# Kernel tuning notes

Hardware: AMD Instinct MI355X
Metric: run time of the kernel (lower is better)

## Reference

```python
import jax, jax.numpy as jnp
import numpy as np

SIGMA = 1e-4            # df_cone_height
PENALIZE_OUTSIDE = True
POINT2PLANE = False
EPS = 1e-12


def _tri_frame(tris):
    """tris: [..., 3, 3] -> centroid c [...,3], unit normal n [...,3], circum-radius r [...]."""
    v0, v1, v2 = tris[..., 0, :], tris[..., 1, :], tris[..., 2, :]
    c = (v0 + v1 + v2) / 3.0
    n = jnp.cross(v1 - v0, v2 - v0)
    n = n / jnp.maximum(jnp.linalg.norm(n, axis=-1, keepdims=True), EPS)
    r = jnp.sqrt(jnp.maximum(jnp.maximum(jnp.sum((v0 - c) ** 2, -1),
                                         jnp.sum((v1 - c) ** 2, -1)),
                             jnp.sum((v2 - c) ** 2, -1)))
    return c, n, r


def _cone_psi(points, c, n, r):
    """Conic distance-field value of each point w.r.t. a triangle cone.
    points: [..., 3, 3] (3 vertices), c/n: [..., 3], r: [...]. Returns [..., 3].
    Cone: axis = triangle normal through centroid, base radius r, height SIGMA.
    """
    u = points - c[..., None, :]                       # [..., 3v, 3]
    h = jnp.einsum('...vk,...k->...v', u, n)           # signed height along normal
    rho = jnp.linalg.norm(u - h[..., None] * n[..., None, :], axis=-1)  # radial dist
    radial = jnp.maximum(1.0 - rho / jnp.maximum(r[..., None], EPS), 0.0)
    if PENALIZE_OUTSIDE:
        axial = jnp.maximum(SIGMA - h, 0.0)            # also penalize thin band above surface
    else:
        axial = jnp.maximum(-h, 0.0)                   # only true penetration (below surface)
    return radial * axial


def setup_inputs() -> dict:
    key = jax.random.key(0)
    B, V, F, C = 8, 10475, 20908, 262144
    k1, k2, k3, k4 = jax.random.split(key, 4)
    vertices = jax.random.normal(k1, (B, V, 3), dtype=jnp.float32)
    faces = jax.random.randint(k2, (F, 3), 0, V)
    idxs = jax.random.randint(k3, (B, C, 2), 0, F)
    invalid = jax.random.uniform(k4, (B, C)) < 0.2     # padded (-1) collision slots
    collision_idxs = jnp.where(invalid[..., None], -1, idxs)
    return {"vertices": vertices, "faces": faces, "collision_idxs": collision_idxs}


def reference(vertices, faces, collision_idxs):
    # triangles: [B, F, 3, 3]
    triangles = jnp.take(vertices, faces, axis=1)
    recv_idx = collision_idxs[..., 0]                  # [B, C]
    intr_idx = collision_idxs[..., 1]
    valid = (recv_idx >= 0) & (intr_idx >= 0)
    # irregular gather of colliding triangle pairs: [B, C, 3, 3]
    recv = jnp.take_along_axis(triangles, jnp.clip(recv_idx, 0)[..., None, None], axis=1)
    intr = jnp.take_along_axis(triangles, jnp.clip(intr_idx, 0)[..., None, None], axis=1)
    rc, rn, rr = _tri_frame(recv)
    ic, inn, ir = _tri_frame(intr)
    psi_i = _cone_psi(intr, rc, rn, rr)                # intruder verts in receiver cone [B,C,3]
    psi_r = _cone_psi(recv, ic, inn, ir)               # receiver verts in intruder cone
    # penetration vector per vertex = -psi * n (unit normal) -> squared norm = psi^2
    per_pair = jnp.sum(psi_i ** 2 + psi_r ** 2, axis=-1)  # [B, C]
    loss = jnp.sum(jnp.where(valid, per_pair, 0.0), axis=1)  # [B]
    # original returns 0.0 when no collision index is >= 0
    return jnp.where(jnp.any(valid), loss, jnp.zeros_like(loss))
```

## Files before the change

kernel.cpp:

```cpp
#include <hip/hip_runtime.h>

#define SIGMA_C 1e-4f
#define EPS_C   1e-12f
#define GPT     4

struct V3 { float x, y, z; };
typedef float v2f __attribute__((ext_vector_type(2)));

__device__ __forceinline__ V3 v3sub(V3 a, V3 b) { return {a.x - b.x, a.y - b.y, a.z - b.z}; }
__device__ __forceinline__ float v3dot(V3 a, V3 b) { return a.x * b.x + a.y * b.y + a.z * b.z; }
__device__ __forceinline__ V3 v3cross(V3 a, V3 b) {
    return {a.y * b.z - a.z * b.y,
            a.z * b.x - a.x * b.z,
            a.x * b.y - a.y * b.x};
}
__device__ __forceinline__ int imax0(int x) { return x > 0 ? x : 0; }

__device__ __forceinline__ void tri_frame(const V3 v[3], V3& c, V3& n, float& r) {
    const float third = 1.0f / 3.0f;
    c.x = (v[0].x + v[1].x + v[2].x) * third;
    c.y = (v[0].y + v[1].y + v[2].y) * third;
    c.z = (v[0].z + v[1].z + v[2].z) * third;
    V3 e1 = v3sub(v[1], v[0]);
    V3 e2 = v3sub(v[2], v[0]);
    n = v3cross(e1, e2);
    float nn = sqrtf(v3dot(n, n));
    float inv = 1.0f / fmaxf(nn, EPS_C);
    n.x *= inv; n.y *= inv; n.z *= inv;
    V3 d0 = v3sub(v[0], c), d1 = v3sub(v[1], c), d2 = v3sub(v[2], c);
    float m = fmaxf(fmaxf(v3dot(d0, d0), v3dot(d1, d1)), v3dot(d2, d2));
    r = sqrtf(m);
}

__device__ __forceinline__ float cone_psi2(const V3 p[3], V3 c, V3 n, float r) {
    float inv_r = 1.0f / fmaxf(r, EPS_C);
    float s = 0.0f;
#pragma unroll
    for (int i = 0; i < 3; ++i) {
        V3 u = v3sub(p[i], c);
        float h = v3dot(u, n);
        V3 w = {u.x - h * n.x, u.y - h * n.y, u.z - h * n.z};
        float rho = sqrtf(v3dot(w, w));
        float radial = fmaxf(1.0f - rho * inv_r, 0.0f);
        float axial = fmaxf(SIGMA_C - h, 0.0f);
        float psi = radial * axial;
        s += psi * psi;
    }
    return s;
}

struct RecF { V3 p0, p1, p2, c, n; float r; };

__device__ __forceinline__ void decode_rec8(float4 q, RecF& o) {
    int4 d = *(int4*)&q;
    v2f t0 = __builtin_amdgcn_cvt_pk_f32_fp8(d.x, false);
    v2f t1 = __builtin_amdgcn_cvt_pk_f32_fp8(d.x, true);
    v2f t2 = __builtin_amdgcn_cvt_pk_f32_fp8(d.y, false);
    v2f t3 = __builtin_amdgcn_cvt_pk_f32_fp8(d.y, true);
    v2f t4 = __builtin_amdgcn_cvt_pk_f32_fp8(d.z, false);
    v2f t5 = __builtin_amdgcn_cvt_pk_f32_fp8(d.z, true);
    v2f t6 = __builtin_amdgcn_cvt_pk_f32_fp8(d.w, false);
    v2f t7 = __builtin_amdgcn_cvt_pk_f32_fp8(d.w, true);
    o.p0 = {t0.x, t0.y, t1.x};
    o.p1 = {t1.y, t2.x, t2.y};
    o.p2 = {t3.x, t3.y, t4.x};
    o.c  = {t4.y, t5.x, t5.y};
    o.n  = {t6.x, t6.y, t7.x};
    o.r  = t7.y;
}

__device__ __forceinline__ float compute_pair8(float4 R, float4 I, float w) {
    RecF rr, ii;
    decode_rec8(R, rr);
    decode_rec8(I, ii);
    V3 rp[3] = {rr.p0, rr.p1, rr.p2};
    V3 ip[3] = {ii.p0, ii.p1, ii.p2};
    return w * (cone_psi2(ip, rr.c, rr.n, rr.r) + cone_psi2(rp, ii.c, ii.n, ii.r));
}

__global__ void precompute_tri_8(const float* __restrict__ verts,
                                 const int*   __restrict__ faces,
                                 float4* __restrict__ table,
                                 float* __restrict__ out,
                                 int V, int F, int B) {
    if (blockIdx.x == 0 && threadIdx.x < (unsigned)B)
        out[threadIdx.x] = 0.0f;

    const int b = blockIdx.x % B;
    const int chunk = blockIdx.x / B;
    const int f0 = (chunk * blockDim.x + threadIdx.x) * 2;
    if (f0 >= F) return;
    const int nf = (f0 + 1 < F) ? 2 : 1;

    const float* vb = verts + (size_t)b * (size_t)V * 3u;

    int ia[6];
#pragma unroll
    for (int j = 0; j < 3; ++j) ia[j] = faces[3 * f0 + j];
#pragma unroll
    for (int j = 0; j < 3; ++j) ia[3 + j] = faces[3 * (f0 + nf - 1) + j];

    V3 pv[6];
#pragma unroll
    for (int j = 0; j < 6; ++j) {
        int vi = ia[j];
        pv[j] = {vb[3 * vi + 0], vb[3 * vi + 1], vb[3 * vi + 2]};
    }

#pragma unroll
    for (int k = 0; k < 2; ++k) {
        if (k >= nf) break;
        V3 v[3] = {pv[3 * k], pv[3 * k + 1], pv[3 * k + 2]};
        V3 c, n; float r;
        tri_frame(v, c, n, r);
        int d0 = 0, d1 = 0, d2 = 0, d3 = 0;
        d0 = __builtin_amdgcn_cvt_pk_fp8_f32(v[0].x, v[0].y, d0, false);
        d0 = __builtin_amdgcn_cvt_pk_fp8_f32(v[0].z, v[1].x, d0, true);
        d1 = __builtin_amdgcn_cvt_pk_fp8_f32(v[1].y, v[1].z, d1, false);
        d1 = __builtin_amdgcn_cvt_pk_fp8_f32(v[2].x, v[2].y, d1, true);
        d2 = __builtin_amdgcn_cvt_pk_fp8_f32(v[2].z, c.x, d2, false);
        d2 = __builtin_amdgcn_cvt_pk_fp8_f32(c.y, c.z, d2, true);
        d3 = __builtin_amdgcn_cvt_pk_fp8_f32(n.x, n.y, d3, false);
        d3 = __builtin_amdgcn_cvt_pk_fp8_f32(n.z, r, d3, true);
        int4 rec = {d0, d1, d2, d3};
        table[(size_t)b * F + (f0 + k)] = *(float4*)&rec;
    }
}

__device__ __forceinline__ void gather_group8(const float4* __restrict__ tb, int4 q,
                                              float4 G[4], float w[2]) {
    w[0] = ((q.x | q.y) >= 0) ? 1.0f : 0.0f;
    w[1] = ((q.z | q.w) >= 0) ? 1.0f : 0.0f;
    G[0] = tb[imax0(q.x)];
    G[1] = tb[imax0(q.y)];
    G[2] = tb[imax0(q.z)];
    G[3] = tb[imax0(q.w)];
}
__device__ __forceinline__ float compute_group8(const float4 G[4], const float w[2]) {
    return compute_pair8(G[0], G[1], w[0]) + compute_pair8(G[2], G[3], w[1]);
}

__global__ void __launch_bounds__(256)
pair_kernel_f8(const float4* __restrict__ table,
               const int4*  __restrict__ coll4,
               float* __restrict__ out,
               int F, int C4, int B) {
    const int b = blockIdx.x % B;
    const int chunk = blockIdx.x / B;
    const int4* cb = coll4 + (size_t)b * C4;
    const float4* tb = table + (size_t)b * (size_t)F;
    const int base = chunk * (256 * GPT) + threadIdx.x;

    float acc = 0.0f;
    float4 GA[4], GB[4];
    float wA[2], wB[2];
    int4 q_even, q_odd;
    {
        int g0 = base, g1 = base + 256;
        q_even = (g0 < C4) ? cb[g0] : make_int4(-1, -1, -1, -1);
        q_odd  = (g1 < C4) ? cb[g1] : make_int4(-1, -1, -1, -1);
        gather_group8(tb, q_even, GA, wA);
    }
#pragma unroll
    for (int i = 0; i < GPT; ++i) {
        if ((i & 1) == 0) {
            if (i + 2 < GPT) {
                int g = base + (i + 2) * 256;
                q_even = (g < C4) ? cb[g] : make_int4(-1, -1, -1, -1);
            }
            if (i + 1 < GPT) gather_group8(tb, q_odd, GB, wB);
            acc += compute_group8(GA, wA);
        } else {
            if (i + 2 < GPT) {
                int g = base + (i + 2) * 256;
                q_odd = (g < C4) ? cb[g] : make_int4(-1, -1, -1, -1);
            }
            if (i + 1 < GPT) gather_group8(tb, q_even, GA, wA);
            acc += compute_group8(GB, wB);
        }
    }

#pragma unroll
    for (int off = 32; off > 0; off >>= 1)
        acc += __shfl_down(acc, off, 64);

    __shared__ float red[4];
    int lane = threadIdx.x & 63;
    int wid  = threadIdx.x >> 6;
    if (lane == 0) red[wid] = acc;
    __syncthreads();
    if (threadIdx.x == 0) {
        float s = red[0] + red[1] + red[2] + red[3];
        atomicAdd(&out[b], s);
    }
}

__global__ void interp_zero(float* out, int n) {
    int i = blockIdx.x * blockDim.x + threadIdx.x;
    if (i < n) out[i] = 0.0f;
}
__global__ void pair_kernel_gather(const float* __restrict__ verts,
                                   const int*   __restrict__ faces,
                                   const int2*  __restrict__ coll,
                                   float* __restrict__ out, int V, int C) {
    const int b = blockIdx.y;
    const float* vb = verts + (size_t)b * (size_t)V * 3u;
    const int2* cb = coll + (size_t)b * (size_t)C;
    float acc = 0.0f;
    const int stride = gridDim.x * blockDim.x;
    for (int c = blockIdx.x * blockDim.x + threadIdx.x; c < C; c += stride) {
        int2 idx = cb[c];
        if ((idx.x | idx.y) >= 0) {
            const int* fr = faces + 3 * idx.x;
            const int* fi = faces + 3 * idx.y;
            V3 tr[3], ti[3];
#pragma unroll
            for (int j = 0; j < 3; ++j) {
                int vr = fr[j];
                tr[j] = {vb[3 * vr + 0], vb[3 * vr + 1], vb[3 * vr + 2]};
                int vi = fi[j];
                ti[j] = {vb[3 * vi + 0], vb[3 * vi + 1], vb[3 * vi + 2]};
            }
            V3 rc, rn; float rr;
            tri_frame(tr, rc, rn, rr);
            V3 ic, in_; float ir;
            tri_frame(ti, ic, in_, ir);
            acc += cone_psi2(ti, rc, rn, rr);
            acc += cone_psi2(tr, ic, in_, ir);
        }
    }
#pragma unroll
    for (int off = 32; off > 0; off >>= 1)
        acc += __shfl_down(acc, off, 64);
    __shared__ float red[16];
    int lane = threadIdx.x & 63, wid = threadIdx.x >> 6;
    if (lane == 0) red[wid] = acc;
    __syncthreads();
    if (threadIdx.x == 0) {
        float s = 0.0f;
        int nw = blockDim.x >> 6;
        for (int i = 0; i < nw; ++i) s += red[i];
        atomicAdd(&out[b], s);
    }
}

extern "C" void kernel_launch(void* const* d_in, const int* in_sizes, int n_in,
                              void* d_out, int out_size, void* d_ws, size_t ws_size,
                              hipStream_t stream) {
    const float* verts = (const float*)d_in[0];
    const int*   faces = (const int*)d_in[1];
    float* out = (float*)d_out;

    const int B = out_size;
    const int V = in_sizes[0] / (3 * B);
    const int F = in_sizes[1] / 3;
    const int C = in_sizes[2] / (2 * B);

    const size_t table_bytes = (size_t)B * (size_t)F * 16u;

    if (ws_size >= table_bytes && (C % 2) == 0) {
        float4* table = (float4*)d_ws;

        const int pchunks = (F + 511) / 512;
        precompute_tri_8<<<dim3(pchunks * B), dim3(256), 0, stream>>>(
            verts, faces, table, out, V, F, B);

        const int C4 = C / 2;
        const int per_block = 256 * GPT;
        const int chunks = (C4 + per_block - 1) / per_block;
        pair_kernel_f8<<<dim3(chunks * B), dim3(256), 0, stream>>>(
            table, (const int4*)d_in[2], out, F, C4, B);
    } else {
        interp_zero<<<1, 64, 0, stream>>>(out, B);
        pair_kernel_gather<<<dim3(256, B), dim3(256), 0, stream>>>(
            verts, faces, (const int2*)d_in[2], out, V, C);
    }
}
```

Baseline: 30.60 us.

## Fuse triangle precompute and pair loss into one cooperative kernel with grid sync

Merges the per-triangle table build and the pair-gather loss into a single cooperative kernel. A grid-wide barrier separates the two phases, so one launch and its inter-kernel gap are removed. Each block builds a slice of the fp8 triangle table before the barrier, then processes its pair chunk. The grid is chunks*B = 128*8 = 1024 blocks of 256 threads, so cooperative launch needs 4 resident blocks per CU across 256 CUs, which is why launch bounds request 4. If the cooperative launch fails it falls back to the two-kernel path, and the grid sync itself adds cost.

```diff
diff --git a/kernel.cpp b/kernel.cpp
--- a/kernel.cpp
+++ b/kernel.cpp
@@ -1,4 +1,7 @@
 #include <hip/hip_runtime.h>
+#include <hip/hip_cooperative_groups.h>
+
+namespace cg = cooperative_groups;
 
 #define SIGMA_C 1e-4f
 #define EPS_C   1e-12f
@@ -78,55 +81,6 @@
     return w * (cone_psi2(ip, rr.c, rr.n, rr.r) + cone_psi2(rp, ii.c, ii.n, ii.r));
 }
 
-__global__ void precompute_tri_8(const float* __restrict__ verts,
-                                 const int*   __restrict__ faces,
-                                 float4* __restrict__ table,
-                                 float* __restrict__ out,
-                                 int V, int F, int B) {
-    if (blockIdx.x == 0 && threadIdx.x < (unsigned)B)
-        out[threadIdx.x] = 0.0f;
-
-    const int b = blockIdx.x % B;
-    const int chunk = blockIdx.x / B;
-    const int f0 = (chunk * blockDim.x + threadIdx.x) * 2;
-    if (f0 >= F) return;
-    const int nf = (f0 + 1 < F) ? 2 : 1;
-
-    const float* vb = verts + (size_t)b * (size_t)V * 3u;
-
-    int ia[6];
-#pragma unroll
-    for (int j = 0; j < 3; ++j) ia[j] = faces[3 * f0 + j];
-#pragma unroll
-    for (int j = 0; j < 3; ++j) ia[3 + j] = faces[3 * (f0 + nf - 1) + j];
-
-    V3 pv[6];
-#pragma unroll
-    for (int j = 0; j < 6; ++j) {
-        int vi = ia[j];
-        pv[j] = {vb[3 * vi + 0], vb[3 * vi + 1], vb[3 * vi + 2]};
-    }
-
-#pragma unroll
-    for (int k = 0; k < 2; ++k) {
-        if (k >= nf) break;
-        V3 v[3] = {pv[3 * k], pv[3 * k + 1], pv[3 * k + 2]};
-        V3 c, n; float r;
-        tri_frame(v, c, n, r);
-        int d0 = 0, d1 = 0, d2 = 0, d3 = 0;
-        d0 = __builtin_amdgcn_cvt_pk_fp8_f32(v[0].x, v[0].y, d0, false);
-        d0 = __builtin_amdgcn_cvt_pk_fp8_f32(v[0].z, v[1].x, d0, true);
-        d1 = __builtin_amdgcn_cvt_pk_fp8_f32(v[1].y, v[1].z, d1, false);
-        d1 = __builtin_amdgcn_cvt_pk_fp8_f32(v[2].x, v[2].y, d1, true);
-        d2 = __builtin_amdgcn_cvt_pk_fp8_f32(v[2].z, c.x, d2, false);
-        d2 = __builtin_amdgcn_cvt_pk_fp8_f32(c.y, c.z, d2, true);
-        d3 = __builtin_amdgcn_cvt_pk_fp8_f32(n.x, n.y, d3, false);
-        d3 = __builtin_amdgcn_cvt_pk_fp8_f32(n.z, r, d3, true);
-        int4 rec = {d0, d1, d2, d3};
-        table[(size_t)b * F + (f0 + k)] = *(float4*)&rec;
-    }
-}
-
 __device__ __forceinline__ void gather_group8(const float4* __restrict__ tb, int4 q,
                                               float4 G[4], float w[2]) {
     w[0] = ((q.x | q.y) >= 0) ? 1.0f : 0.0f;
@@ -138,6 +92,133 @@
 }
 __device__ __forceinline__ float compute_group8(const float4 G[4], const float w[2]) {
     return compute_pair8(G[0], G[1], w[0]) + compute_pair8(G[2], G[3], w[1]);
+}
+
+__global__ void __launch_bounds__(256, 4)
+fused_f8(const float* __restrict__ verts,
+         const int*   __restrict__ faces,
+         const int4*  __restrict__ coll4,
+         float4* __restrict__ table,
+         float* __restrict__ out,
+         int V, int F, int C4, int B, int FPB) {
+    const int b = blockIdx.x % B;
+    const int chunk = blockIdx.x / B;
+
+    if (blockIdx.x == 0 && threadIdx.x < (unsigned)B)
+        out[threadIdx.x] = 0.0f;
+
+    {
+        const float* vb = verts + (size_t)b * (size_t)V * 3u;
+        const int fbeg = chunk * FPB;
+        const int fend = min(fbeg + FPB, F);
+        for (int f = fbeg + (int)threadIdx.x; f < fend; f += 256) {
+            int i0 = faces[3 * f + 0];
+            int i1 = faces[3 * f + 1];
+            int i2 = faces[3 * f + 2];
+            V3 v[3];
+            v[0] = {vb[3 * i0 + 0], vb[3 * i0 + 1], vb[3 * i0 + 2]};
+            v[1] = {vb[3 * i1 + 0], vb[3 * i1 + 1], vb[3 * i1 + 2]};
+            v[2] = {vb[3 * i2 + 0], vb[3 * i2 + 1], vb[3 * i2 + 2]};
+            V3 c, n; float r;
+            tri_frame(v, c, n, r);
+            int d0 = 0, d1 = 0, d2 = 0, d3 = 0;
+            d0 = __builtin_amdgcn_cvt_pk_fp8_f32(v[0].x, v[0].y, d0, false);
+            d0 = __builtin_amdgcn_cvt_pk_fp8_f32(v[0].z, v[1].x, d0, true);
+            d1 = __builtin_amdgcn_cvt_pk_fp8_f32(v[1].y, v[1].z, d1, false);
+            d1 = __builtin_amdgcn_cvt_pk_fp8_f32(v[2].x, v[2].y, d1, true);
+            d2 = __builtin_amdgcn_cvt_pk_fp8_f32(v[2].z, c.x, d2, false);
+            d2 = __builtin_amdgcn_cvt_pk_fp8_f32(c.y, c.z, d2, true);
+            d3 = __builtin_amdgcn_cvt_pk_fp8_f32(n.x, n.y, d3, false);
+            d3 = __builtin_amdgcn_cvt_pk_fp8_f32(n.z, r, d3, true);
+            int4 rec = {d0, d1, d2, d3};
+            table[(size_t)b * F + f] = *(float4*)&rec;
+        }
+    }
+
+    cg::this_grid().sync();
+
+    const int4* cb = coll4 + (size_t)b * C4;
+    const float4* tb = table + (size_t)b * (size_t)F;
+    const int base = chunk * (256 * GPT) + (int)threadIdx.x;
+
+    float acc = 0.0f;
+    float4 GA[4], GB[4];
+    float wA[2], wB[2];
+    int4 q_even, q_odd;
+    {
+        int g0 = base, g1 = base + 256;
+        q_even = (g0 < C4) ? cb[g0] : make_int4(-1, -1, -1, -1);
+        q_odd  = (g1 < C4) ? cb[g1] : make_int4(-1, -1, -1, -1);
+        gather_group8(tb, q_even, GA, wA);
+    }
+#pragma unroll
+    for (int i = 0; i < GPT; ++i) {
+        if ((i & 1) == 0) {
+            if (i + 2 < GPT) {
+                int g = base + (i + 2) * 256;
+                q_even = (g < C4) ? cb[g] : make_int4(-1, -1, -1, -1);
+            }
+            if (i + 1 < GPT) gather_group8(tb, q_odd, GB, wB);
+            acc += compute_group8(GA, wA);
+        } else {
+            if (i + 2 < GPT) {
+                int g = base + (i + 2) * 256;
+                q_odd = (g < C4) ? cb[g] : make_int4(-1, -1, -1, -1);
+            }
+            if (i + 1 < GPT) gather_group8(tb, q_even, GA, wA);
+            acc += compute_group8(GB, wB);
+        }
+    }
+
+#pragma unroll
+    for (int off = 32; off > 0; off >>= 1)
+        acc += __shfl_down(acc, off, 64);
+
+    __shared__ float red[4];
+    int lane = threadIdx.x & 63;
+    int wid  = threadIdx.x >> 6;
+    if (lane == 0) red[wid] = acc;
+    __syncthreads();
+    if (threadIdx.x == 0) {
+        float s = red[0] + red[1] + red[2] + red[3];
+        atomicAdd(&out[b], s);
+    }
+}
+
+__global__ void precompute_tri_8(const float* __restrict__ verts,
+                                 const int*   __restrict__ faces,
+                                 float4* __restrict__ table,
+                                 float* __restrict__ out,
+                                 int V, int F, int B) {
+    if (blockIdx.x == 0 && threadIdx.x < (unsigned)B)
+        out[threadIdx.x] = 0.0f;
+
+    const int b = blockIdx.x % B;
+    const int chunk = blockIdx.x / B;
+    const int f = chunk * blockDim.x + threadIdx.x;
+    if (f >= F) return;
+
+    const float* vb = verts + (size_t)b * (size_t)V * 3u;
+    int i0 = faces[3 * f + 0];
+    int i1 = faces[3 * f + 1];
+    int i2 = faces[3 * f + 2];
+    V3 v[3];
+    v[0] = {vb[3 * i0 + 0], vb[3 * i0 + 1], vb[3 * i0 + 2]};
+    v[1] = {vb[3 * i1 + 0], vb[3 * i1 + 1], vb[3 * i1 + 2]};
+    v[2] = {vb[3 * i2 + 0], vb[3 * i2 + 1], vb[3 * i2 + 2]};
+    V3 c, n; float r;
+    tri_frame(v, c, n, r);
+    int d0 = 0, d1 = 0, d2 = 0, d3 = 0;
+    d0 = __builtin_amdgcn_cvt_pk_fp8_f32(v[0].x, v[0].y, d0, false);
+    d0 = __builtin_amdgcn_cvt_pk_fp8_f32(v[0].z, v[1].x, d0, true);
+    d1 = __builtin_amdgcn_cvt_pk_fp8_f32(v[1].y, v[1].z, d1, false);
+    d1 = __builtin_amdgcn_cvt_pk_fp8_f32(v[2].x, v[2].y, d1, true);
+    d2 = __builtin_amdgcn_cvt_pk_fp8_f32(v[2].z, c.x, d2, false);
+    d2 = __builtin_amdgcn_cvt_pk_fp8_f32(c.y, c.z, d2, true);
+    d3 = __builtin_amdgcn_cvt_pk_fp8_f32(n.x, n.y, d3, false);
+    d3 = __builtin_amdgcn_cvt_pk_fp8_f32(n.z, r, d3, true);
+    int4 rec = {d0, d1, d2, d3};
+    table[(size_t)b * F + f] = *(float4*)&rec;
 }
 
 __global__ void __launch_bounds__(256)
@@ -257,19 +338,28 @@
     const int C = in_sizes[2] / (2 * B);
 
     const size_t table_bytes = (size_t)B * (size_t)F * 16u;
-
-    if (ws_size >= table_bytes && (C % 2) == 0) {
+    const int per_block_pairs = 256 * GPT * 2;
+
+    if (ws_size >= table_bytes && (C % per_block_pairs) == 0) {
         float4* table = (float4*)d_ws;
-
-        const int pchunks = (F + 511) / 512;
+        const int4* coll4 = (const int4*)d_in[2];
+        int C4 = C / 2;
+        int chunks = C / per_block_pairs;
+        int grid = chunks * B;
+        int FPB = (F + chunks - 1) / chunks;
+
+        void* tblv = (void*)table;
+        void* args[] = {(void*)&verts, (void*)&faces, (void*)&coll4, (void*)&tblv,
+                        (void*)&out, (void*)&V, (void*)&F, (void*)&C4, (void*)&B, (void*)&FPB};
+        hipError_t err = hipLaunchCooperativeKernel(
+            (const void*)fused_f8, dim3(grid), dim3(256), args, 0, stream);
+        if (err == hipSuccess) return;
+
+        const int pchunks = (F + 255) / 256;
         precompute_tri_8<<<dim3(pchunks * B), dim3(256), 0, stream>>>(
             verts, faces, table, out, V, F, B);
-
-        const int C4 = C / 2;
-        const int per_block = 256 * GPT;
-        const int chunks = (C4 + per_block - 1) / per_block;
         pair_kernel_f8<<<dim3(chunks * B), dim3(256), 0, stream>>>(
-            table, (const int4*)d_in[2], out, F, C4, B);
+            table, coll4, out, F, C4, B);
     } else {
         interp_zero<<<1, 64, 0, stream>>>(out, B);
         pair_kernel_gather<<<dim3(256, B), dim3(256), 0, stream>>>(
```

Result: slower. 117.1 us (+282.7%).

## Use one face per thread in precompute and two groups per thread in pair kernel

Applied to the files above, without the earlier changes.

The precompute kernel now handles one triangle per thread instead of two, doubling its grid. The pair kernel drops the four-group software-pipelined loop and has each thread process just two groups, with collision indices read through nontemporal loads. This doubles the pair-kernel block count to raise parallelism and expose more gathers in flight at once. The cost is more per-block reduction and atomic work, and the fast path now requires C to be a multiple of 1024.

```diff
diff --git a/kernel.cpp b/kernel.cpp
--- a/kernel.cpp
+++ b/kernel.cpp
@@ -2,10 +2,10 @@
 
 #define SIGMA_C 1e-4f
 #define EPS_C   1e-12f
-#define GPT     4
 
 struct V3 { float x, y, z; };
 typedef float v2f __attribute__((ext_vector_type(2)));
+typedef int   v4i __attribute__((ext_vector_type(4)));
 
 __device__ __forceinline__ V3 v3sub(V3 a, V3 b) { return {a.x - b.x, a.y - b.y, a.z - b.z}; }
 __device__ __forceinline__ float v3dot(V3 a, V3 b) { return a.x * b.x + a.y * b.y + a.z * b.z; }
@@ -78,55 +78,6 @@
     return w * (cone_psi2(ip, rr.c, rr.n, rr.r) + cone_psi2(rp, ii.c, ii.n, ii.r));
 }
 
-__global__ void precompute_tri_8(const float* __restrict__ verts,
-                                 const int*   __restrict__ faces,
-                                 float4* __restrict__ table,
-                                 float* __restrict__ out,
-                                 int V, int F, int B) {
-    if (blockIdx.x == 0 && threadIdx.x < (unsigned)B)
-        out[threadIdx.x] = 0.0f;
-
-    const int b = blockIdx.x % B;
-    const int chunk = blockIdx.x / B;
-    const int f0 = (chunk * blockDim.x + threadIdx.x) * 2;
-    if (f0 >= F) return;
-    const int nf = (f0 + 1 < F) ? 2 : 1;
-
-    const float* vb = verts + (size_t)b * (size_t)V * 3u;
-
-    int ia[6];
-#pragma unroll
-    for (int j = 0; j < 3; ++j) ia[j] = faces[3 * f0 + j];
-#pragma unroll
-    for (int j = 0; j < 3; ++j) ia[3 + j] = faces[3 * (f0 + nf - 1) + j];
-
-    V3 pv[6];
-#pragma unroll
-    for (int j = 0; j < 6; ++j) {
-        int vi = ia[j];
-        pv[j] = {vb[3 * vi + 0], vb[3 * vi + 1], vb[3 * vi + 2]};
-    }
-
-#pragma unroll
-    for (int k = 0; k < 2; ++k) {
-        if (k >= nf) break;
-        V3 v[3] = {pv[3 * k], pv[3 * k + 1], pv[3 * k + 2]};
-        V3 c, n; float r;
-        tri_frame(v, c, n, r);
-        int d0 = 0, d1 = 0, d2 = 0, d3 = 0;
-        d0 = __builtin_amdgcn_cvt_pk_fp8_f32(v[0].x, v[0].y, d0, false);
-        d0 = __builtin_amdgcn_cvt_pk_fp8_f32(v[0].z, v[1].x, d0, true);
-        d1 = __builtin_amdgcn_cvt_pk_fp8_f32(v[1].y, v[1].z, d1, false);
-        d1 = __builtin_amdgcn_cvt_pk_fp8_f32(v[2].x, v[2].y, d1, true);
-        d2 = __builtin_amdgcn_cvt_pk_fp8_f32(v[2].z, c.x, d2, false);
-        d2 = __builtin_amdgcn_cvt_pk_fp8_f32(c.y, c.z, d2, true);
-        d3 = __builtin_amdgcn_cvt_pk_fp8_f32(n.x, n.y, d3, false);
-        d3 = __builtin_amdgcn_cvt_pk_fp8_f32(n.z, r, d3, true);
-        int4 rec = {d0, d1, d2, d3};
-        table[(size_t)b * F + (f0 + k)] = *(float4*)&rec;
-    }
-}
-
 __device__ __forceinline__ void gather_group8(const float4* __restrict__ tb, int4 q,
                                               float4 G[4], float w[2]) {
     w[0] = ((q.x | q.y) >= 0) ? 1.0f : 0.0f;
@@ -138,6 +89,47 @@
 }
 __device__ __forceinline__ float compute_group8(const float4 G[4], const float w[2]) {
     return compute_pair8(G[0], G[1], w[0]) + compute_pair8(G[2], G[3], w[1]);
+}
+
+__device__ __forceinline__ int4 nt_load_i4(const int4* p) {
+    v4i v = __builtin_nontemporal_load((const v4i*)p);
+    return make_int4(v.x, v.y, v.z, v.w);
+}
+
+__global__ void precompute_tri_8(const float* __restrict__ verts,
+                                 const int*   __restrict__ faces,
+                                 float4* __restrict__ table,
+                                 float* __restrict__ out,
+                                 int V, int F, int B) {
+    if (blockIdx.x == 0 && threadIdx.x < (unsigned)B)
+        out[threadIdx.x] = 0.0f;
+
+    const int b = blockIdx.x % B;
+    const int chunk = blockIdx.x / B;
+    const int f = chunk * blockDim.x + threadIdx.x;
+    if (f >= F) return;
+
+    const float* vb = verts + (size_t)b * (size_t)V * 3u;
+    int i0 = faces[3 * f + 0];
+    int i1 = faces[3 * f + 1];
+    int i2 = faces[3 * f + 2];
+    V3 v[3];
+    v[0] = {vb[3 * i0 + 0], vb[3 * i0 + 1], vb[3 * i0 + 2]};
+    v[1] = {vb[3 * i1 + 0], vb[3 * i1 + 1], vb[3 * i1 + 2]};
+    v[2] = {vb[3 * i2 + 0], vb[3 * i2 + 1], vb[3 * i2 + 2]};
+    V3 c, n; float r;
+    tri_frame(v, c, n, r);
+    int d0 = 0, d1 = 0, d2 = 0, d3 = 0;
+    d0 = __builtin_amdgcn_cvt_pk_fp8_f32(v[0].x, v[0].y, d0, false);
+    d0 = __builtin_amdgcn_cvt_pk_fp8_f32(v[0].z, v[1].x, d0, true);
+    d1 = __builtin_amdgcn_cvt_pk_fp8_f32(v[1].y, v[1].z, d1, false);
+    d1 = __builtin_amdgcn_cvt_pk_fp8_f32(v[2].x, v[2].y, d1, true);
+    d2 = __builtin_amdgcn_cvt_pk_fp8_f32(v[2].z, c.x, d2, false);
+    d2 = __builtin_amdgcn_cvt_pk_fp8_f32(c.y, c.z, d2, true);
+    d3 = __builtin_amdgcn_cvt_pk_fp8_f32(n.x, n.y, d3, false);
+    d3 = __builtin_amdgcn_cvt_pk_fp8_f32(n.z, r, d3, true);
+    int4 rec = {d0, d1, d2, d3};
+    table[(size_t)b * F + f] = *(float4*)&rec;
 }
 
 __global__ void __launch_bounds__(256)
@@ -149,36 +141,20 @@
     const int chunk = blockIdx.x / B;
     const int4* cb = coll4 + (size_t)b * C4;
     const float4* tb = table + (size_t)b * (size_t)F;
-    const int base = chunk * (256 * GPT) + threadIdx.x;
-
-    float acc = 0.0f;
+    const int base = chunk * (256 * 2) + (int)threadIdx.x;
+
+    int g0 = base, g1 = base + 256;
+    int4 q_even = (g0 < C4) ? nt_load_i4(cb + g0) : make_int4(-1, -1, -1, -1);
+    int4 q_odd  = (g1 < C4) ? nt_load_i4(cb + g1) : make_int4(-1, -1, -1, -1);
+
     float4 GA[4], GB[4];
     float wA[2], wB[2];
-    int4 q_even, q_odd;
-    {
-        int g0 = base, g1 = base + 256;
-        q_even = (g0 < C4) ? cb[g0] : make_int4(-1, -1, -1, -1);
-        q_odd  = (g1 < C4) ? cb[g1] : make_int4(-1, -1, -1, -1);
-        gather_group8(tb, q_even, GA, wA);
-    }
-#pragma unroll
-    for (int i = 0; i < GPT; ++i) {
-        if ((i & 1) == 0) {
-            if (i + 2 < GPT) {
-                int g = base + (i + 2) * 256;
-                q_even = (g < C4) ? cb[g] : make_int4(-1, -1, -1, -1);
-            }
-            if (i + 1 < GPT) gather_group8(tb, q_odd, GB, wB);
-            acc += compute_group8(GA, wA);
-        } else {
-            if (i + 2 < GPT) {
-                int g = base + (i + 2) * 256;
-                q_odd = (g < C4) ? cb[g] : make_int4(-1, -1, -1, -1);
-            }
-            if (i + 1 < GPT) gather_group8(tb, q_even, GA, wA);
-            acc += compute_group8(GB, wB);
-        }
-    }
+
+    gather_group8(tb, q_even, GA, wA);
+    gather_group8(tb, q_odd,  GB, wB);
+
+    float acc = compute_group8(GA, wA);
+    acc += compute_group8(GB, wB);
 
 #pragma unroll
     for (int off = 32; off > 0; off >>= 1)
@@ -257,19 +233,20 @@
     const int C = in_sizes[2] / (2 * B);
 
     const size_t table_bytes = (size_t)B * (size_t)F * 16u;
-
-    if (ws_size >= table_bytes && (C % 2) == 0) {
+    const int per_block_pairs = 256 * 2 * 2;
+
+    if (ws_size >= table_bytes && (C % per_block_pairs) == 0) {
         float4* table = (float4*)d_ws;
-
-        const int pchunks = (F + 511) / 512;
+        const int4* coll4 = (const int4*)d_in[2];
+        const int C4 = C / 2;
+
+        const int pchunks = (F + 255) / 256;
         precompute_tri_8<<<dim3(pchunks * B), dim3(256), 0, stream>>>(
             verts, faces, table, out, V, F, B);
 
-        const int C4 = C / 2;
-        const int per_block = 256 * GPT;
-        const int chunks = (C4 + per_block - 1) / per_block;
+        const int chunks = C / per_block_pairs;
         pair_kernel_f8<<<dim3(chunks * B), dim3(256), 0, stream>>>(
-            table, (const int4*)d_in[2], out, F, C4, B);
+            table, coll4, out, F, C4, B);
     } else {
         interp_zero<<<1, 64, 0, stream>>>(out, B);
         pair_kernel_gather<<<dim3(256, B), dim3(256), 0, stream>>>(
```

Result: slower. 41.21 us (+34.6%).
